# Kernel optimization log

Measured on AMD Instinct MI355X. Metric: run time of the kernel, lower is better.

## Reference

```python
import jax, jax.numpy as jnp
import numpy as np


def setup_inputs() -> dict:
    key = jax.random.key(0)
    k1, k2, k3, k4, k5 = jax.random.split(key, 5)
    N, V, C = 4096, 4, 256
    desc = jax.random.normal(k1, (N, V, C), dtype=jnp.float32)
    sf = jax.random.normal(k2, (N, V, C), dtype=jnp.float32)
    T = jax.random.normal(k3, (V, 4, 4), dtype=jnp.float32)
    W_rec = jax.random.normal(k4, (C, C), dtype=jnp.float32) * (1.0 / np.sqrt(C))
    W_T = jax.random.normal(k5, (32, C), dtype=jnp.float32) * (1.0 / np.sqrt(32))
    return {"desc": desc, "sf": sf, "T": T, "W_rec": W_rec, "W_T": W_T}


def reference(desc, sf, T, W_rec, W_T):
    # desc, sf: [N, V, C]; T: [V, 4, 4]
    N, V, C = desc.shape
    # F.normalize(desc, dim=2)
    dn = desc / jnp.maximum(jnp.linalg.norm(desc, axis=2, keepdims=True), 1e-12)
    ar = jnp.arange(N)
    loss_total = jnp.zeros((), dtype=desc.dtype)
    count = jnp.zeros((), dtype=desc.dtype)
    for i in range(V):
        for j in range(V):
            if i == j:
                continue
            di = dn[:, i, :]  # [N, C]
            dj = dn[:, j, :]  # [N, C]
            sim = di @ dj.T   # [N, N]
            idx_ij = jnp.argmax(sim, axis=1)
            idx_ji = jnp.argmax(sim, axis=0)
            mutual = (idx_ji[idx_ij] == ar)  # [N] bool, mutual nearest neighbors
            # kpnet.reconstruction(desc_i, T_i, T_j): linear, transform-conditioned
            rel = jnp.concatenate([T[i].ravel(), T[j].ravel()])  # [32]
            sf_recon = di @ W_rec + rel @ W_T  # [N, C]
            # torch.no_grad() block -> stop_gradient
            prob = jax.nn.softmax(sim, axis=1)
            sf_j_soft = jax.lax.stop_gradient(prob @ sf[:, j, :])  # [N, C]
            m = mutual.astype(desc.dtype)[:, None]  # [N, 1]
            n_sel = jnp.sum(m)
            sq = jnp.sum(((sf_recon - sf_j_soft) ** 2) * m)
            pair_loss = sq / jnp.maximum(n_sel * C, 1.0)  # masked MSE (mean over selected elems)
            valid = (n_sel > 0).astype(desc.dtype)
            loss_total = loss_total + valid * pair_loss
            count = count + valid
    return jnp.where(count > 0, loss_total / jnp.maximum(count, 1.0), 0.0 * jnp.sum(desc))
```

## Files before the change

kernel.cpp:

```cpp
#include <hip/hip_runtime.h>
#include <math.h>

#define N_ 4096
#define V_ 4
#define C_ 256

typedef __attribute__((ext_vector_type(8))) short bf16x8;
typedef __attribute__((ext_vector_type(4))) float f32x4;
typedef unsigned long long u64;

#define OFF_R      0ull
#define OFF_DNHI   16777216ull
#define OFF_DNLO   25165824ull
#define OFF_SFT    33554432ull
#define OFF_E      37748736ull
#define OFF_ET     88080384ull
#define OFF_WTH    138412032ull
#define OFF_WTL    138543104ull
#define OFF_ROWPK  138674176ull
#define OFF_COLPK  138870784ull
#define OFF_ROWSM  139067392ull
#define OFF_COLSM  139165696ull
#define OFF_RELWT  139264000ull
#define OFF_SQ     139280384ull
#define OFF_CNT    139280448ull

__device__ __forceinline__ unsigned short f2bf(float x) {
    unsigned int u = __float_as_uint(x);
    u += 0x7fffu + ((u >> 16) & 1u);
    return (unsigned short)(u >> 16);
}
__device__ __forceinline__ float bf2f(unsigned short h) {
    return __uint_as_float(((unsigned int)h) << 16);
}
__device__ __forceinline__ f32x4 mfma16(bf16x8 a, bf16x8 b, f32x4 c) {
    return __builtin_amdgcn_mfma_f32_16x16x32_bf16(a, b, c, 0, 0, 0);
}
__device__ __forceinline__ unsigned int pk4fp8(float x0, float x1, float x2, float x3) {
    int w = 0;
    w = __builtin_amdgcn_cvt_pk_fp8_f32(x0, x1, w, false);
    w = __builtin_amdgcn_cvt_pk_fp8_f32(x2, x3, w, true);
    return (unsigned int)w;
}

__global__ void normalize_k(const float* __restrict__ desc,
                            unsigned short* __restrict__ dnh, unsigned short* __restrict__ dnl) {
    int row = blockIdx.x;
    int n = row >> 2, v = row & 3;
    int c = threadIdx.x;
    float x = desc[(size_t)row * C_ + c];
    __shared__ float red[256];
    red[c] = x * x;
    __syncthreads();
    for (int s = 128; s > 0; s >>= 1) {
        if (c < s) red[c] += red[c + s];
        __syncthreads();
    }
    float inv = 1.0f / fmaxf(sqrtf(red[0]), 1e-12f);
    float y = x * inv;
    size_t o = ((size_t)v * N_ + n) * C_ + c;
    unsigned short h = f2bf(y);
    dnh[o] = h;
    dnl[o] = f2bf(y - bf2f(h));
}

__global__ void wrecT_k(const float* __restrict__ W, unsigned short* __restrict__ WTh,
                        unsigned short* __restrict__ WTl) {
    __shared__ float Tt[64 * 65];
    int k0 = blockIdx.x * 64, c0 = blockIdx.y * 64;
    int t = threadIdx.x;
    int kr = t >> 2, cq = (t & 3) * 16;
    const float* src = W + (size_t)(k0 + kr) * C_ + c0 + cq;
    for (int u = 0; u < 16; ++u) Tt[(cq + u) * 65 + kr] = src[u];
    __syncthreads();
    int cr = t >> 2, kq = (t & 3) * 16;
    unsigned short th[16] __attribute__((aligned(16)));
    unsigned short tl[16] __attribute__((aligned(16)));
    for (int u = 0; u < 16; ++u) {
        float x = Tt[cr * 65 + kq + u];
        unsigned short h = f2bf(x);
        th[u] = h; tl[u] = f2bf(x - bf2f(h));
    }
    size_t o = (size_t)(c0 + cr) * C_ + k0 + kq;
    *(uint4*)(WTh + o) = *(const uint4*)th;
    *(uint4*)(WTh + o + 8) = *(const uint4*)(th + 8);
    *(uint4*)(WTl + o) = *(const uint4*)tl;
    *(uint4*)(WTl + o + 8) = *(const uint4*)(tl + 8);
}

__global__ __launch_bounds__(256) void rmatmul_k(
    const unsigned short* __restrict__ Ah, const unsigned short* __restrict__ Al,
    const unsigned short* __restrict__ Bh, const unsigned short* __restrict__ Bl,
    float* __restrict__ R) {
    __shared__ unsigned short smem[4 * 128 * 40];
    unsigned short* sAh = smem;
    unsigned short* sAl = sAh + 128 * 40;
    unsigned short* sBh = sAl + 128 * 40;
    unsigned short* sBl = sBh + 128 * 40;
    int tid = threadIdx.x;
    int c0 = blockIdx.x * 128, m0 = blockIdx.y * 128;
    int w = tid >> 6, l = tid & 63, wm = w & 1, wn = w >> 1;
    int mr = l & 15, q = l >> 4;
    f32x4 acc[4][4];
#pragma unroll
    for (int a = 0; a < 4; ++a)
#pragma unroll
        for (int b = 0; b < 4; ++b)
#pragma unroll
            for (int u = 0; u < 4; ++u) acc[a][b][u] = 0.f;
    int r = tid >> 1, h = (tid & 1) * 16;
    for (int k0 = 0; k0 < C_; k0 += 32) {
        size_t ga = (size_t)(m0 + r) * C_ + k0 + h;
        size_t gb = (size_t)(c0 + r) * C_ + k0 + h;
        uint4 a0 = *(const uint4*)(Ah + ga);
        uint4 a1 = *(const uint4*)(Ah + ga + 8);
        uint4 a2 = *(const uint4*)(Al + ga);
        uint4 a3 = *(const uint4*)(Al + ga + 8);
        uint4 b0 = *(const uint4*)(Bh + gb);
        uint4 b1 = *(const uint4*)(Bh + gb + 8);
        uint4 b2 = *(const uint4*)(Bl + gb);
        uint4 b3 = *(const uint4*)(Bl + gb + 8);
        *(uint4*)(sAh + r * 40 + h)     = a0;
        *(uint4*)(sAh + r * 40 + h + 8) = a1;
        *(uint4*)(sAl + r * 40 + h)     = a2;
        *(uint4*)(sAl + r * 40 + h + 8) = a3;
        *(uint4*)(sBh + r * 40 + h)     = b0;
        *(uint4*)(sBh + r * 40 + h + 8) = b1;
        *(uint4*)(sBl + r * 40 + h)     = b2;
        *(uint4*)(sBl + r * 40 + h + 8) = b3;
        __syncthreads();
        bf16x8 fah[4], fal[4], fbh[4], fbl[4];
#pragma unroll
        for (int ti = 0; ti < 4; ++ti) {
            int row = wm * 64 + ti * 16 + mr;
            fah[ti] = *(const bf16x8*)(sAh + row * 40 + q * 8);
            fal[ti] = *(const bf16x8*)(sAl + row * 40 + q * 8);
        }
#pragma unroll
        for (int tj = 0; tj < 4; ++tj) {
            int row = wn * 64 + tj * 16 + mr;
            fbh[tj] = *(const bf16x8*)(sBh + row * 40 + q * 8);
            fbl[tj] = *(const bf16x8*)(sBl + row * 40 + q * 8);
        }
#pragma unroll
        for (int ti = 0; ti < 4; ++ti)
#pragma unroll
            for (int tj = 0; tj < 4; ++tj) acc[ti][tj] = mfma16(fah[ti], fbh[tj], acc[ti][tj]);
#pragma unroll
        for (int ti = 0; ti < 4; ++ti)
#pragma unroll
            for (int tj = 0; tj < 4; ++tj) acc[ti][tj] = mfma16(fah[ti], fbl[tj], acc[ti][tj]);
#pragma unroll
        for (int ti = 0; ti < 4; ++ti)
#pragma unroll
            for (int tj = 0; tj < 4; ++tj) acc[ti][tj] = mfma16(fal[ti], fbh[tj], acc[ti][tj]);
        __syncthreads();
    }
#pragma unroll
    for (int ti = 0; ti < 4; ++ti)
#pragma unroll
        for (int tj = 0; tj < 4; ++tj) {
            int c = c0 + wn * 64 + tj * 16 + mr;
#pragma unroll
            for (int rg = 0; rg < 4; ++rg) {
                int m = m0 + wm * 64 + ti * 16 + q * 4 + rg;
                R[(size_t)m * C_ + c] = acc[ti][tj][rg];
            }
        }
}

__global__ void relwt_k(const float* __restrict__ T, const float* __restrict__ WT,
                        float* __restrict__ relwt) {
    int p = blockIdx.x; int i = p >> 2, j = p & 3;
    if (i == j) return;
    int c = threadIdx.x;
    float acc = 0.f;
    for (int k = 0; k < 16; ++k) acc += T[i * 16 + k] * WT[(size_t)k * C_ + c];
    for (int k = 0; k < 16; ++k) acc += T[j * 16 + k] * WT[(size_t)(16 + k) * C_ + c];
    relwt[(size_t)p * C_ + c] = acc;
}

__global__ void sfT_k(const float* __restrict__ sf, unsigned char* __restrict__ sf8T) {
    __shared__ float Tt[64 * 65];
    int n0 = blockIdx.x * 64, c0 = blockIdx.y * 64, v = blockIdx.z;
    int t = threadIdx.x;
    int nr = t >> 2, cq = (t & 3) * 16;
    const float* src = sf + ((size_t)(n0 + nr) * V_ + v) * C_ + c0 + cq;
    for (int u = 0; u < 16; ++u) Tt[(cq + u) * 65 + nr] = src[u];
    __syncthreads();
    int cr = t >> 2, nq = (t & 3) * 16;
    unsigned int wb[4];
#pragma unroll
    for (int g = 0; g < 4; ++g) {
        const float* p = Tt + cr * 65 + nq + g * 4;
        wb[g] = pk4fp8(p[0], p[1], p[2], p[3]);
    }
    unsigned char* dst = sf8T + ((size_t)v * C_ + c0 + cr) * N_ + n0 + nq;
    *(uint4*)dst = make_uint4(wb[0], wb[1], wb[2], wb[3]);
}

__global__ void zero_k(u64* rowPk, u64* colPk, float* rowSm, float* colSm,
                       float* sq, int* cnt) {
    int idx = blockIdx.x * 256 + threadIdx.x;
    rowPk[idx] = 0ull; colPk[idx] = 0ull;
    rowSm[idx] = 0.f;  colSm[idx] = 0.f;
    if (idx < 16) { sq[idx] = 0.f; cnt[idx] = 0; }
}

__global__ __launch_bounds__(256) void sim_mfma_k(
    const unsigned short* __restrict__ dnh, const unsigned short* __restrict__ dnl,
    int ipack, int jpack, unsigned char* __restrict__ E8b, unsigned char* __restrict__ ET8b,
    u64* __restrict__ rowPkB, float* __restrict__ rowSmB,
    u64* __restrict__ colPkB, float* __restrict__ colSmB, int slotBase) {
    __shared__ unsigned char smem[36864];
    __shared__ float sRedM[256];
    __shared__ int   sRedA[256];
    __shared__ float sRedS[256];
    unsigned short* sAh = (unsigned short*)smem;
    unsigned short* sAl = sAh + 64 * 72;
    unsigned short* sBh = sAl + 64 * 72;
    unsigned short* sBl = sBh + 64 * 72;
    float* S = (float*)smem;

    int zp = blockIdx.z;
    int iv = (ipack >> (8 * zp)) & 15;
    int jv = (jpack >> (8 * zp)) & 15;
    const unsigned short* Ahi = dnh + (size_t)iv * N_ * C_;
    const unsigned short* Alo = dnl + (size_t)iv * N_ * C_;
    const unsigned short* Bhi = dnh + (size_t)jv * N_ * C_;
    const unsigned short* Blo = dnl + (size_t)jv * N_ * C_;
    unsigned char* E8  = E8b  + (size_t)zp * N_ * N_;
    unsigned char* ET8 = ET8b + (size_t)zp * N_ * N_;
    int slot = slotBase + zp;
    u64*   rowPk = rowPkB + (size_t)slot * N_;
    float* rowSm = rowSmB + (size_t)slot * N_;
    u64*   colPk = colPkB + (size_t)slot * N_;
    float* colSm = colSmB + (size_t)slot * N_;

    int tid = threadIdx.x;
    int m0 = blockIdx.y * 64, n0 = blockIdx.x * 64;
    int w = tid >> 6, l = tid & 63;
    int wm = w & 1, wn = w >> 1;
    int mr = l & 15, q = l >> 4;

    f32x4 acc[2][2];
#pragma unroll
    for (int a = 0; a < 2; ++a)
#pragma unroll
        for (int b = 0; b < 2; ++b)
#pragma unroll
            for (int u = 0; u < 4; ++u) acc[a][b][u] = 0.f;

    int r = tid >> 2;
    int k8 = (tid & 3) * 8;

    for (int k0 = 0; k0 < C_; k0 += 64) {
        size_t ga = (size_t)(m0 + r) * C_ + k0 + k8;
        size_t gb = (size_t)(n0 + r) * C_ + k0 + k8;
        uint4 a0 = *(const uint4*)(Ahi + ga);
        uint4 a1 = *(const uint4*)(Ahi + ga + 32);
        uint4 a2 = *(const uint4*)(Alo + ga);
        uint4 a3 = *(const uint4*)(Alo + ga + 32);
        uint4 b0 = *(const uint4*)(Bhi + gb);
        uint4 b1 = *(const uint4*)(Bhi + gb + 32);
        uint4 b2 = *(const uint4*)(Blo + gb);
        uint4 b3 = *(const uint4*)(Blo + gb + 32);
        *(uint4*)(sAh + r * 72 + k8)      = a0;
        *(uint4*)(sAh + r * 72 + k8 + 32) = a1;
        *(uint4*)(sAl + r * 72 + k8)      = a2;
        *(uint4*)(sAl + r * 72 + k8 + 32) = a3;
        *(uint4*)(sBh + r * 72 + k8)      = b0;
        *(uint4*)(sBh + r * 72 + k8 + 32) = b1;
        *(uint4*)(sBl + r * 72 + k8)      = b2;
        *(uint4*)(sBl + r * 72 + k8 + 32) = b3;
        __syncthreads();
#pragma unroll
        for (int ks = 0; ks < 64; ks += 32) {
            bf16x8 ah[2], al[2], bh[2], bl[2];
#pragma unroll
            for (int ti = 0; ti < 2; ++ti) {
                int mrow = wm * 32 + ti * 16 + mr;
                ah[ti] = *(const bf16x8*)(sAh + mrow * 72 + ks + q * 8);
                al[ti] = *(const bf16x8*)(sAl + mrow * 72 + ks + q * 8);
            }
#pragma unroll
            for (int tj = 0; tj < 2; ++tj) {
                int nrow = wn * 32 + tj * 16 + mr;
                bh[tj] = *(const bf16x8*)(sBh + nrow * 72 + ks + q * 8);
                bl[tj] = *(const bf16x8*)(sBl + nrow * 72 + ks + q * 8);
            }
#pragma unroll
            for (int ti = 0; ti < 2; ++ti)
#pragma unroll
                for (int tj = 0; tj < 2; ++tj) {
                    acc[ti][tj] = mfma16(ah[ti], bh[tj], acc[ti][tj]);
                    acc[ti][tj] = mfma16(ah[ti], bl[tj], acc[ti][tj]);
                    acc[ti][tj] = mfma16(al[ti], bh[tj], acc[ti][tj]);
                }
        }
        __syncthreads();
    }

#pragma unroll
    for (int ti = 0; ti < 2; ++ti)
#pragma unroll
        for (int tj = 0; tj < 2; ++tj)
#pragma unroll
            for (int rg = 0; rg < 4; ++rg)
                S[(wm * 32 + ti * 16 + q * 4 + rg) * 65 + wn * 32 + tj * 16 + mr] =
                    __expf(acc[ti][tj][rg]);
    __syncthreads();

    {
        int rr = tid >> 2, q4 = tid & 3;
        float mx = -1e30f; int ag = 0; float sm = 0.f;
        for (int cc = 0; cc < 16; ++cc) {
            int c = q4 * 16 + cc;
            float v = S[rr * 65 + c];
            sm += v;
            if (v > mx) { mx = v; ag = c; }
        }
        sRedM[tid] = mx; sRedA[tid] = ag; sRedS[tid] = sm;
    }
    __syncthreads();
    if (tid < 64) {
        float mx = -1e30f; int ag = 0; float sm = 0.f;
        for (int qq = 0; qq < 4; ++qq) {
            float v = sRedM[tid * 4 + qq];
            if (v > mx) { mx = v; ag = sRedA[tid * 4 + qq]; }
            sm += sRedS[tid * 4 + qq];
        }
        u64 pk = ((u64)__float_as_uint(mx) << 32) | (u64)(0xFFFFFFFFu - (unsigned)(n0 + ag));
        atomicMax(rowPk + m0 + tid, pk);
        atomicAdd(rowSm + m0 + tid, sm);
    }
    __syncthreads();
    {
        int cc = tid >> 2, q4 = tid & 3;
        float mx = -1e30f; int ag = 0; float sm = 0.f;
        for (int rr = 0; rr < 16; ++rr) {
            int rrr = q4 * 16 + rr;
            float v = S[rrr * 65 + cc];
            sm += v;
            if (v > mx) { mx = v; ag = rrr; }
        }
        sRedM[tid] = mx; sRedA[tid] = ag; sRedS[tid] = sm;
    }
    __syncthreads();
    if (tid < 64) {
        float mx = -1e30f; int ag = 0; float sm = 0.f;
        for (int qq = 0; qq < 4; ++qq) {
            float v = sRedM[tid * 4 + qq];
            if (v > mx) { mx = v; ag = sRedA[tid * 4 + qq]; }
            sm += sRedS[tid * 4 + qq];
        }
        u64 pk = ((u64)__float_as_uint(mx) << 32) | (u64)(0xFFFFFFFFu - (unsigned)(m0 + ag));
        atomicMax(colPk + n0 + tid, pk);
        atomicAdd(colSm + n0 + tid, sm);
    }
    {
        int r2 = tid >> 2, cq = (tid & 3) * 16;
        unsigned int wb[4];
#pragma unroll
        for (int g = 0; g < 4; ++g) {
            const float* p = S + r2 * 65 + cq + g * 4;
            wb[g] = pk4fp8(p[0], p[1], p[2], p[3]);
        }
        *(uint4*)(E8 + (size_t)(m0 + r2) * N_ + n0 + cq) = make_uint4(wb[0], wb[1], wb[2], wb[3]);
    }
    {
        int n2 = tid >> 2, mq = (tid & 3) * 16;
        unsigned int wb[4];
#pragma unroll
        for (int g = 0; g < 4; ++g) {
            wb[g] = pk4fp8(S[(mq + g * 4 + 0) * 65 + n2], S[(mq + g * 4 + 1) * 65 + n2],
                           S[(mq + g * 4 + 2) * 65 + n2], S[(mq + g * 4 + 3) * 65 + n2]);
        }
        *(uint4*)(ET8 + (size_t)(n0 + n2) * N_ + m0 + mq) = make_uint4(wb[0], wb[1], wb[2], wb[3]);
    }
}

__global__ __launch_bounds__(256) void p2_k(
    const unsigned char* __restrict__ E8b, const unsigned char* __restrict__ ET8b,
    const unsigned char* __restrict__ sf8T, int ipack, int jpack,
    const u64* __restrict__ rowPkB, const float* __restrict__ rowSmB,
    const u64* __restrict__ colPkB, const float* __restrict__ colSmB, int slotBase,
    const float* __restrict__ R, const float* __restrict__ relwt,
    float* __restrict__ pairSq, int* __restrict__ pairCnt) {
    __shared__ unsigned char sA[32 * 144];
    __shared__ unsigned char sB[64 * 144];
    __shared__ float red[256];
    __shared__ int   mutS[32];
    __shared__ float invS[32];
    int tid = threadIdx.x;
    int zp = blockIdx.y;
    int iv = (ipack >> (8 * zp)) & 15;
    int jv = (jpack >> (8 * zp)) & 15;
    int slot = slotBase + zp;
    int lin = blockIdx.x;
    int xcd = lin & 7, slotx = lin >> 3;
    int grp = xcd + 8 * (slotx >> 2);
    int ct = slotx & 3;
    int mt = grp & 127, d = grp >> 7;
    const unsigned char* A = (d ? ET8b : E8b) + (size_t)zp * N_ * N_;
    const unsigned char* B = sf8T + (size_t)(d ? iv : jv) * C_ * N_;
    const u64* faPk = (d ? colPkB : rowPkB) + (size_t)slot * N_;
    const u64* baPk = (d ? rowPkB : colPkB) + (size_t)slot * N_;
    const float* sumE = (d ? colSmB : rowSmB) + (size_t)slot * N_;
    const float* Rr = R + (size_t)(d ? jv : iv) * N_ * C_;
    int pid = d ? (jv * 4 + iv) : (iv * 4 + jv);
    int c0 = ct * 64, m0 = mt * 32;
    int w = tid >> 6, l = tid & 63, wm = w & 1, wn = w >> 1;
    int mr = l & 15, q = l >> 4;
    if (tid < 32) {
        int y = m0 + tid;
        unsigned faIdx = 0xFFFFFFFFu - (unsigned)(faPk[y] & 0xFFFFFFFFull);
        unsigned baIdx = 0xFFFFFFFFu - (unsigned)(baPk[faIdx] & 0xFFFFFFFFull);
        mutS[tid] = (baIdx == (unsigned)y) ? 1 : 0;
        invS[tid] = 1.0f / sumE[y];
    }
    f32x4 acc[2];
#pragma unroll
    for (int b = 0; b < 2; ++b)
#pragma unroll
        for (int u = 0; u < 4; ++u) acc[b][u] = 0.f;

    int ra = tid >> 3, ka = (tid & 7) * 16;
    int rb = tid >> 2, kb = (tid & 3) * 32;
    const unsigned char* Arow = A + (size_t)(m0 + ra) * N_;
    const unsigned char* Brow = B + (size_t)(c0 + rb) * N_;
    uint4 pa  = *(const uint4*)(Arow + ka);
    uint4 pb0 = *(const uint4*)(Brow + kb);
    uint4 pb1 = *(const uint4*)(Brow + kb + 16);
    for (int k0 = 0; k0 < N_; k0 += 128) {
        *(uint4*)(sA + ra * 144 + ka)      = pa;
        *(uint4*)(sB + rb * 144 + kb)      = pb0;
        *(uint4*)(sB + rb * 144 + kb + 16) = pb1;
        __syncthreads();
        int kn = k0 + 128;
        if (kn < N_) {
            pa  = *(const uint4*)(Arow + kn + ka);
            pb0 = *(const uint4*)(Brow + kn + kb);
            pb1 = *(const uint4*)(Brow + kn + kb + 16);
        }
#pragma unroll
        for (int ksub = 0; ksub < 128; ksub += 32) {
            long af = *(const long*)(sA + (wm * 16 + mr) * 144 + ksub + q * 8);
            long b0 = *(const long*)(sB + (wn * 32 + mr) * 144 + ksub + q * 8);
            long b1 = *(const long*)(sB + (wn * 32 + 16 + mr) * 144 + ksub + q * 8);
            acc[0] = __builtin_amdgcn_mfma_f32_16x16x32_fp8_fp8(af, b0, acc[0], 0, 0, 0);
            acc[1] = __builtin_amdgcn_mfma_f32_16x16x32_fp8_fp8(af, b1, acc[1], 0, 0, 0);
        }
        __syncthreads();
    }
    const float* rw = relwt + (size_t)pid * C_;
    float local = 0.f;
#pragma unroll
    for (int tj = 0; tj < 2; ++tj) {
        int c = c0 + wn * 32 + tj * 16 + mr;
        float rwc = rw[c];
#pragma unroll
        for (int rg = 0; rg < 4; ++rg) {
            int ml = wm * 16 + q * 4 + rg;
            if (mutS[ml]) {
                int m = m0 + ml;
                float soft = acc[tj][rg] * invS[ml];
                float dv = Rr[(size_t)m * C_ + c] + rwc - soft;
                local += dv * dv;
            }
        }
    }
    red[tid] = local;
    __syncthreads();
    for (int s = 128; s > 0; s >>= 1) {
        if (tid < s) red[tid] += red[tid + s];
        __syncthreads();
    }
    if (tid == 0) {
        atomicAdd(pairSq + pid, red[0]);
        if (ct == 0) {
            int cnt = 0;
            for (int u = 0; u < 32; ++u) cnt += mutS[u];
            atomicAdd(pairCnt + pid, cnt);
        }
    }
}

__global__ void final_k(const float* __restrict__ sq, const int* __restrict__ cnt,
                        float* __restrict__ out) {
    if (threadIdx.x == 0 && blockIdx.x == 0) {
        float loss = 0.f, count = 0.f;
        for (int p = 0; p < 16; ++p) {
            int i = p >> 2, j = p & 3;
            if (i == j) continue;
            float ns = (float)cnt[p];
            if (ns > 0.f) { loss += sq[p] / fmaxf(ns * (float)C_, 1.0f); count += 1.f; }
        }
        out[0] = (count > 0.f) ? loss / count : 0.f;
    }
}

extern "C" void kernel_launch(void* const* d_in, const int* in_sizes, int n_in,
                              void* d_out, int out_size, void* d_ws, size_t ws_size,
                              hipStream_t stream) {
    const float* desc = (const float*)d_in[0];
    const float* sf   = (const float*)d_in[1];
    const float* T    = (const float*)d_in[2];
    const float* Wrec = (const float*)d_in[3];
    const float* WT   = (const float*)d_in[4];
    float* out = (float*)d_out;
    char* ws = (char*)d_ws;

    float*          R     = (float*)(ws + OFF_R);
    unsigned short* dnh   = (unsigned short*)(ws + OFF_DNHI);
    unsigned short* dnl   = (unsigned short*)(ws + OFF_DNLO);
    unsigned char*  sf8T  = (unsigned char*)(ws + OFF_SFT);
    unsigned char*  E8b   = (unsigned char*)(ws + OFF_E);
    unsigned char*  ET8b  = (unsigned char*)(ws + OFF_ET);
    unsigned short* WTh   = (unsigned short*)(ws + OFF_WTH);
    unsigned short* WTl   = (unsigned short*)(ws + OFF_WTL);
    u64*   rowPk = (u64*)(ws + OFF_ROWPK);
    u64*   colPk = (u64*)(ws + OFF_COLPK);
    float* rowSm = (float*)(ws + OFF_ROWSM);
    float* colSm = (float*)(ws + OFF_COLSM);
    float* relwt = (float*)(ws + OFF_RELWT);
    float* pairSq = (float*)(ws + OFF_SQ);
    int*   pairCnt = (int*)(ws + OFF_CNT);

    normalize_k<<<N_ * V_, 256, 0, stream>>>(desc, dnh, dnl);
    wrecT_k<<<dim3(4, 4), 256, 0, stream>>>(Wrec, WTh, WTl);
    rmatmul_k<<<dim3(2, 128), 256, 0, stream>>>(dnh, dnl, WTh, WTl, R);
    sfT_k<<<dim3(64, 4, 4), 256, 0, stream>>>(sf, sf8T);
    relwt_k<<<16, 256, 0, stream>>>(T, WT, relwt);
    zero_k<<<96, 256, 0, stream>>>(rowPk, colPk, rowSm, colSm, pairSq, pairCnt);

    const int ip[2] = { 0 | (0 << 8) | (0 << 16), 1 | (1 << 8) | (2 << 16) };
    const int jp[2] = { 1 | (2 << 8) | (3 << 16), 2 | (3 << 8) | (3 << 16) };
    for (int b = 0; b < 2; ++b) {
        sim_mfma_k<<<dim3(64, 64, 3), 256, 0, stream>>>(
            dnh, dnl, ip[b], jp[b], E8b, ET8b, rowPk, rowSm, colPk, colSm, b * 3);
        p2_k<<<dim3(1024, 3), 256, 0, stream>>>(
            E8b, ET8b, sf8T, ip[b], jp[b], rowPk, rowSm, colPk, colSm, b * 3,
            R, relwt, pairSq, pairCnt);
    }
    final_k<<<1, 64, 0, stream>>>(pairSq, pairCnt, out);
}
```

Before: 562.7 us.

## Enlarge p2_k output tile to 64x128 with 2x4 MFMA register blocking

The prob@sf GEMM kernel moves from a 32x64 output tile per block to a 64x128 tile, with each wave computing a 2x4 grid of 16x16 MFMA accumulators instead of 1x2. This raises arithmetic intensity and cuts redundant reads of the fp8 E matrix, which was previously re-read by four column tiles and is now re-read by two. The K step shrinks from 128 to 64 and the grid drops from 3072 to 768 blocks, and the XCD-aware block index remapping is removed. The risk is lower occupancy from more accumulator registers and fewer blocks to fill the GPU.

Result: faster. 511.1 us (-9.2%).

```diff
diff --git a/kernel.cpp b/kernel.cpp
--- a/kernel.cpp
+++ b/kernel.cpp
@@ -387,21 +387,17 @@
     const u64* __restrict__ colPkB, const float* __restrict__ colSmB, int slotBase,
     const float* __restrict__ R, const float* __restrict__ relwt,
     float* __restrict__ pairSq, int* __restrict__ pairCnt) {
-    __shared__ unsigned char sA[32 * 144];
-    __shared__ unsigned char sB[64 * 144];
+    __shared__ unsigned char sA[64 * 80];
+    __shared__ unsigned char sB[128 * 80];
     __shared__ float red[256];
-    __shared__ int   mutS[32];
-    __shared__ float invS[32];
+    __shared__ int   mutS[64];
+    __shared__ float invS[64];
     int tid = threadIdx.x;
-    int zp = blockIdx.y;
+    int ct = blockIdx.x & 1, mt = blockIdx.x >> 1;
+    int d = blockIdx.y & 1, zp = blockIdx.y >> 1;
     int iv = (ipack >> (8 * zp)) & 15;
     int jv = (jpack >> (8 * zp)) & 15;
     int slot = slotBase + zp;
-    int lin = blockIdx.x;
-    int xcd = lin & 7, slotx = lin >> 3;
-    int grp = xcd + 8 * (slotx >> 2);
-    int ct = slotx & 3;
-    int mt = grp & 127, d = grp >> 7;
     const unsigned char* A = (d ? ET8b : E8b) + (size_t)zp * N_ * N_;
     const unsigned char* B = sf8T + (size_t)(d ? iv : jv) * C_ * N_;
     const u64* faPk = (d ? colPkB : rowPkB) + (size_t)slot * N_;
@@ -409,67 +405,79 @@
     const float* sumE = (d ? colSmB : rowSmB) + (size_t)slot * N_;
     const float* Rr = R + (size_t)(d ? jv : iv) * N_ * C_;
     int pid = d ? (jv * 4 + iv) : (iv * 4 + jv);
-    int c0 = ct * 64, m0 = mt * 32;
+    int c0 = ct * 128, m0 = mt * 64;
     int w = tid >> 6, l = tid & 63, wm = w & 1, wn = w >> 1;
     int mr = l & 15, q = l >> 4;
-    if (tid < 32) {
+    if (tid < 64) {
         int y = m0 + tid;
         unsigned faIdx = 0xFFFFFFFFu - (unsigned)(faPk[y] & 0xFFFFFFFFull);
         unsigned baIdx = 0xFFFFFFFFu - (unsigned)(baPk[faIdx] & 0xFFFFFFFFull);
         mutS[tid] = (baIdx == (unsigned)y) ? 1 : 0;
         invS[tid] = 1.0f / sumE[y];
     }
-    f32x4 acc[2];
-#pragma unroll
-    for (int b = 0; b < 2; ++b)
-#pragma unroll
-        for (int u = 0; u < 4; ++u) acc[b][u] = 0.f;
-
-    int ra = tid >> 3, ka = (tid & 7) * 16;
-    int rb = tid >> 2, kb = (tid & 3) * 32;
-    const unsigned char* Arow = A + (size_t)(m0 + ra) * N_;
-    const unsigned char* Brow = B + (size_t)(c0 + rb) * N_;
-    uint4 pa  = *(const uint4*)(Arow + ka);
-    uint4 pb0 = *(const uint4*)(Brow + kb);
-    uint4 pb1 = *(const uint4*)(Brow + kb + 16);
-    for (int k0 = 0; k0 < N_; k0 += 128) {
-        *(uint4*)(sA + ra * 144 + ka)      = pa;
-        *(uint4*)(sB + rb * 144 + kb)      = pb0;
-        *(uint4*)(sB + rb * 144 + kb + 16) = pb1;
-        __syncthreads();
-        int kn = k0 + 128;
+    f32x4 acc[2][4];
+#pragma unroll
+    for (int a = 0; a < 2; ++a)
+#pragma unroll
+        for (int b = 0; b < 4; ++b)
+#pragma unroll
+            for (int u = 0; u < 4; ++u) acc[a][b][u] = 0.f;
+
+    int ra = tid >> 2, ka = (tid & 3) * 16;
+    int rb = tid >> 1, kbb = (tid & 1) * 32;
+    const unsigned char* Arow = A + (size_t)(m0 + ra) * N_ + ka;
+    const unsigned char* Brow = B + (size_t)(c0 + rb) * N_ + kbb;
+    uint4 pa  = *(const uint4*)(Arow);
+    uint4 pb0 = *(const uint4*)(Brow);
+    uint4 pb1 = *(const uint4*)(Brow + 16);
+    for (int k0 = 0; k0 < N_; k0 += 64) {
+        *(uint4*)(sA + ra * 80 + ka)       = pa;
+        *(uint4*)(sB + rb * 80 + kbb)      = pb0;
+        *(uint4*)(sB + rb * 80 + kbb + 16) = pb1;
+        __syncthreads();
+        int kn = k0 + 64;
         if (kn < N_) {
-            pa  = *(const uint4*)(Arow + kn + ka);
-            pb0 = *(const uint4*)(Brow + kn + kb);
-            pb1 = *(const uint4*)(Brow + kn + kb + 16);
-        }
-#pragma unroll
-        for (int ksub = 0; ksub < 128; ksub += 32) {
-            long af = *(const long*)(sA + (wm * 16 + mr) * 144 + ksub + q * 8);
-            long b0 = *(const long*)(sB + (wn * 32 + mr) * 144 + ksub + q * 8);
-            long b1 = *(const long*)(sB + (wn * 32 + 16 + mr) * 144 + ksub + q * 8);
-            acc[0] = __builtin_amdgcn_mfma_f32_16x16x32_fp8_fp8(af, b0, acc[0], 0, 0, 0);
-            acc[1] = __builtin_amdgcn_mfma_f32_16x16x32_fp8_fp8(af, b1, acc[1], 0, 0, 0);
+            pa  = *(const uint4*)(Arow + kn);
+            pb0 = *(const uint4*)(Brow + kn);
+            pb1 = *(const uint4*)(Brow + kn + 16);
+        }
+#pragma unroll
+        for (int ksub = 0; ksub < 64; ksub += 32) {
+            long af[2], bf[4];
+#pragma unroll
+            for (int ti = 0; ti < 2; ++ti)
+                af[ti] = *(const long*)(sA + (wm * 32 + ti * 16 + mr) * 80 + ksub + q * 8);
+#pragma unroll
+            for (int tj = 0; tj < 4; ++tj)
+                bf[tj] = *(const long*)(sB + (wn * 64 + tj * 16 + mr) * 80 + ksub + q * 8);
+#pragma unroll
+            for (int ti = 0; ti < 2; ++ti)
+#pragma unroll
+                for (int tj = 0; tj < 4; ++tj)
+                    acc[ti][tj] = __builtin_amdgcn_mfma_f32_16x16x32_fp8_fp8(
+                        af[ti], bf[tj], acc[ti][tj], 0, 0, 0);
         }
         __syncthreads();
     }
     const float* rw = relwt + (size_t)pid * C_;
     float local = 0.f;
 #pragma unroll
-    for (int tj = 0; tj < 2; ++tj) {
-        int c = c0 + wn * 32 + tj * 16 + mr;
-        float rwc = rw[c];
-#pragma unroll
-        for (int rg = 0; rg < 4; ++rg) {
-            int ml = wm * 16 + q * 4 + rg;
-            if (mutS[ml]) {
-                int m = m0 + ml;
-                float soft = acc[tj][rg] * invS[ml];
-                float dv = Rr[(size_t)m * C_ + c] + rwc - soft;
-                local += dv * dv;
+    for (int ti = 0; ti < 2; ++ti)
+#pragma unroll
+        for (int tj = 0; tj < 4; ++tj) {
+            int c = c0 + wn * 64 + tj * 16 + mr;
+            float rwc = rw[c];
+#pragma unroll
+            for (int rg = 0; rg < 4; ++rg) {
+                int ml = wm * 32 + ti * 16 + q * 4 + rg;
+                if (mutS[ml]) {
+                    int m = m0 + ml;
+                    float soft = acc[ti][tj][rg] * invS[ml];
+                    float dv = Rr[(size_t)m * C_ + c] + rwc - soft;
+                    local += dv * dv;
+                }
             }
         }
-    }
     red[tid] = local;
     __syncthreads();
     for (int s = 128; s > 0; s >>= 1) {
@@ -480,7 +488,7 @@
         atomicAdd(pairSq + pid, red[0]);
         if (ct == 0) {
             int cnt = 0;
-            for (int u = 0; u < 32; ++u) cnt += mutS[u];
+            for (int u = 0; u < 64; ++u) cnt += mutS[u];
             atomicAdd(pairCnt + pid, cnt);
         }
     }
@@ -539,7 +547,7 @@
     for (int b = 0; b < 2; ++b) {
         sim_mfma_k<<<dim3(64, 64, 3), 256, 0, stream>>>(
             dnh, dnl, ip[b], jp[b], E8b, ET8b, rowPk, rowSm, colPk, colSm, b * 3);
-        p2_k<<<dim3(1024, 3), 256, 0, stream>>>(
+        p2_k<<<dim3(128, 6), 256, 0, stream>>>(
             E8b, ET8b, sf8T, ip[b], jp[b], rowPk, rowSm, colPk, colSm, b * 3,
             R, relwt, pairSq, pairCnt);
     }
```
